# Kernel tuning notes

Measured on AMD Instinct MI355X. Metric: run time of the kernel, lower is better.

The kernel has to match this reference:

```python
import jax, jax.numpy as jnp
import numpy as np

B, S, D = 4, 2048, 1024  # batch, seq_len, input_dim == output_dim (dk)


def setup_inputs() -> dict:
    key = jax.random.key(0)
    kx, kq, kk, kv = jax.random.split(key, 4)
    # xavier_uniform bound for square [D, D] matrices
    bound = float(np.sqrt(6.0 / (D + D)))
    return {
        "x": jax.random.normal(kx, (B, S, D), dtype=jnp.float32),
        "WQ": jax.random.uniform(kq, (D, D), jnp.float32, -bound, bound),
        "WK": jax.random.uniform(kk, (D, D), jnp.float32, -bound, bound),
        "WV": jax.random.uniform(kv, (D, D), jnp.float32, -bound, bound),
    }


def reference(x, WQ, WK, WV):
    dk = WQ.shape[1]
    q = x @ WQ  # [B, S, dk]
    k = x @ WK
    v = x @ WV
    scores = jnp.einsum("bsd,btd->bst", q, k) / jnp.sqrt(jnp.asarray(dk, x.dtype))
    # causal mask: tril ones -> positions where mask==0 set to -inf
    s = x.shape[1]
    causal = jnp.tril(jnp.ones((s, s), dtype=bool))
    scores = jnp.where(causal[None, :, :], scores, jnp.asarray(-jnp.inf, x.dtype))
    attention = jax.nn.softmax(scores, axis=-1)
    # NOTE: original applies attention_dropout to `scores` post-softmax and
    # discards the result -> dead op; eval-mode output is attention @ v.
    return jnp.einsum("bst,btd->bsd", attention, v)
```

## Files before the change

### kernel.cpp

```cpp
#include <hip/hip_runtime.h>
#include <stdint.h>


typedef unsigned short u16;
typedef __attribute__((ext_vector_type(8))) short shortx8;
typedef __attribute__((ext_vector_type(4))) float floatx4;

static constexpr int BB = 4;
static constexpr int SS = 2048;
static constexpr int DD = 1024;

__device__ __forceinline__ u16 f2bf(float f) {
  union { float f; uint32_t u; } c; c.f = f;
  uint32_t u = c.u;
  return (u16)((u + 0x7fffu + ((u >> 16) & 1u)) >> 16);
}

__device__ __forceinline__ float bfhi2f(uint32_t u) {
  union { uint32_t u; float f; } c; c.u = u & 0xffff0000u; return c.f;
}
__device__ __forceinline__ float bflo2f(uint32_t u) {
  union { uint32_t u; float f; } c; c.u = u << 16; return c.f;
}

#define GLOAD_LDS16(g, l)                                                              \
  __builtin_amdgcn_global_load_lds((const __attribute__((address_space(1))) void*)(g), \
                                   (__attribute__((address_space(3))) void*)(l), 16, 0, 0)

__device__ __forceinline__ void gemm_core_128(
    const u16* __restrict__ A, const u16* __restrict__ Bt,
    int lda, int ldb, int m0, int n0, int kend, floatx4 acc[4][4])
{
  __shared__ u16 lA[128 * 64];
  __shared__ u16 lB[128 * 64];
  const int t = threadIdx.x;
  const int w = t >> 6, l = t & 63;
  const int wm = w >> 1, wn = w & 1;
  const int sr = l >> 3;
  const int scq = ((l & 7) ^ (l >> 3)) * 8;

#pragma unroll
  for (int i = 0; i < 4; ++i)
#pragma unroll
    for (int j = 0; j < 4; ++j)
      acc[i][j] = (floatx4){0.f, 0.f, 0.f, 0.f};

  const u16* Ab = A + (size_t)m0 * lda;
  const u16* Bb = Bt + (size_t)n0 * ldb;

  for (int k0 = 0; k0 < kend; k0 += 64) {
#pragma unroll
    for (int i = 0; i < 4; ++i) {
      const int row = w * 32 + i * 8;
      GLOAD_LDS16(Ab + (size_t)(row + sr) * lda + k0 + scq, &lA[row * 64]);
      GLOAD_LDS16(Bb + (size_t)(row + sr) * ldb + k0 + scq, &lB[row * 64]);
    }
    __syncthreads();

#pragma unroll
    for (int ks = 0; ks < 2; ++ks) {
      const int ca = ((ks * 4 + (l >> 4)) ^ (l & 7)) * 8;
      shortx8 af[4], bf[4];
#pragma unroll
      for (int i = 0; i < 4; ++i)
        af[i] = *(const shortx8*)&lA[(wm * 64 + i * 16 + (l & 15)) * 64 + ca];
#pragma unroll
      for (int i = 0; i < 4; ++i)
        bf[i] = *(const shortx8*)&lB[(wn * 64 + i * 16 + (l & 15)) * 64 + ca];
#pragma unroll
      for (int i = 0; i < 4; ++i)
#pragma unroll
        for (int j = 0; j < 4; ++j)
          acc[i][j] = __builtin_amdgcn_mfma_f32_16x16x32_bf16(af[i], bf[j], acc[i][j], 0, 0, 0);
    }
    __syncthreads();
  }
}

__global__ __launch_bounds__(256) void prep(const float* __restrict__ x,
                                            const float* __restrict__ WQ,
                                            const float* __restrict__ WK,
                                            const float* __restrict__ WV,
                                            u16* __restrict__ xb,
                                            u16* __restrict__ Wt) {
  __shared__ float tile[64][65];
  const int bid = blockIdx.x;
  const int t = threadIdx.x;
  if (bid < 8192) {
    const size_t i = (size_t)bid * 256 + t;
    float4 v = ((const float4*)x)[i];
    ushort4 o;
    o.x = f2bf(v.x); o.y = f2bf(v.y); o.z = f2bf(v.z); o.w = f2bf(v.w);
    ((ushort4*)xb)[i] = o;
    return;
  }
  const int r = bid - 8192;
  const int wsel = r >> 8;
  const int rr = r & 255;
  const int k0 = (rr >> 4) * 64, n0 = (rr & 15) * 64;
  const float* W = wsel == 0 ? WQ : (wsel == 1 ? WK : WV);
  const int tx = t & 63, ty = t >> 6;
#pragma unroll
  for (int i = 0; i < 16; ++i)
    tile[ty + i * 4][tx] = W[(size_t)(k0 + ty + i * 4) * DD + n0 + tx];
  __syncthreads();
  u16* dst = Wt + (size_t)wsel * DD * DD;
#pragma unroll
  for (int i = 0; i < 16; ++i)
    dst[(size_t)(n0 + ty + i * 4) * DD + k0 + tx] = f2bf(tile[tx][ty + i * 4]);
}

__global__ __launch_bounds__(256, 2) void qkv_gemm(const u16* __restrict__ x,
                                                   const u16* __restrict__ Wt,
                                                   u16* __restrict__ Q,
                                                   u16* __restrict__ K,
                                                   u16* __restrict__ Vt) {
  const int m0 = blockIdx.x * 128;
  const int n0t = blockIdx.y * 128;
  floatx4 acc[4][4];
  gemm_core_128(x, Wt, DD, DD, m0, n0t, DD, acc);

  const int t = threadIdx.x, w = t >> 6, l = t & 63;
  const int wm = w >> 1, wn = w & 1;

  if (n0t >= 2048) {
    const int bb = m0 >> 11;
    const int s0 = (m0 & 2047) + wm * 64 + (l >> 4) * 4;
    u16* vt = Vt + (size_t)bb * DD * SS;
#pragma unroll
    for (int i = 0; i < 4; ++i)
#pragma unroll
      for (int j = 0; j < 4; ++j) {
        const int n = (n0t - 2048) + wn * 64 + j * 16 + (l & 15);
        const int s = s0 + i * 16;
        ushort4 o4;
        o4.x = f2bf(acc[i][j][0]);
        o4.y = f2bf(acc[i][j][1]);
        o4.z = f2bf(acc[i][j][2]);
        o4.w = f2bf(acc[i][j][3]);
        *(ushort4*)(vt + (size_t)n * SS + s) = o4;
      }
    return;
  }

  u16* out = (n0t < 1024) ? Q : K;
  const int n0 = n0t & 1023;
#pragma unroll
  for (int i = 0; i < 4; ++i)
#pragma unroll
    for (int j = 0; j < 4; ++j)
#pragma unroll
      for (int r = 0; r < 4; ++r) {
        const int m = m0 + wm * 64 + i * 16 + (l >> 4) * 4 + r;
        const int n = n0 + wn * 64 + j * 16 + (l & 15);
        out[(size_t)m * DD + n] = f2bf(acc[i][j][r]);
      }
}

__global__ __launch_bounds__(256, 2) void scores_gemm(const u16* __restrict__ Q,
                                                      const u16* __restrict__ Kt,
                                                      u16* __restrict__ Scb) {
  const int b = blockIdx.z;
  const int tcode = blockIdx.x;
  int mb = (int)((sqrtf(8.0f * (float)tcode + 1.0f) - 1.0f) * 0.5f);
  while ((mb + 1) * (mb + 2) / 2 <= tcode) ++mb;
  while (mb * (mb + 1) / 2 > tcode) --mb;
  const int nb = tcode - mb * (mb + 1) / 2;
  const int m0 = mb * 128, n0 = nb * 128;

  floatx4 acc[4][4];
  gemm_core_128(Q + (size_t)b * SS * DD, Kt + (size_t)b * SS * DD, DD, DD, m0, n0, DD, acc);

  u16* out = Scb + (size_t)b * SS * SS;
  const int t = threadIdx.x, w = t >> 6, l = t & 63;
  const int wm = w >> 1, wn = w & 1;
#pragma unroll
  for (int i = 0; i < 4; ++i)
#pragma unroll
    for (int j = 0; j < 4; ++j)
#pragma unroll
      for (int r = 0; r < 4; ++r) {
        const int m = m0 + wm * 64 + i * 16 + (l >> 4) * 4 + r;
        const int n = n0 + wn * 64 + j * 16 + (l & 15);
        out[(size_t)m * SS + n] = f2bf(acc[i][j][r] * 0.03125f);
      }
}

__global__ __launch_bounds__(256) void softmax_causal(const u16* __restrict__ Scb,
                                                      u16* __restrict__ P) {
  const int row = blockIdx.x * 4 + (threadIdx.x >> 6);
  const int l = threadIdx.x & 63;
  const int b = row >> 11, i = row & 2047;
  const u16* s = Scb + (size_t)b * SS * SS + (size_t)i * SS;
  u16* p = P + (size_t)b * SS * SS + (size_t)i * SS;
  const int n = i + 1;
  const int jend = (i + 128) & ~127;
  const int nc = (jend + 511) >> 9;

  float v[4][8];
  float mx = -INFINITY;
#pragma unroll
  for (int c = 0; c < 4; ++c) {
    if (c < nc) {
      const int col = c * 512 + l * 8;
      uint4 raw = *(const uint4*)(s + col);
      v[c][0] = bflo2f(raw.x); v[c][1] = bfhi2f(raw.x);
      v[c][2] = bflo2f(raw.y); v[c][3] = bfhi2f(raw.y);
      v[c][4] = bflo2f(raw.z); v[c][5] = bfhi2f(raw.z);
      v[c][6] = bflo2f(raw.w); v[c][7] = bfhi2f(raw.w);
#pragma unroll
      for (int e = 0; e < 8; ++e) {
        v[c][e] = (col + e < n) ? v[c][e] : -INFINITY;
        mx = fmaxf(mx, v[c][e]);
      }
    }
  }
#pragma unroll
  for (int o = 32; o > 0; o >>= 1) mx = fmaxf(mx, __shfl_xor(mx, o, 64));

  float sum = 0.f;
#pragma unroll
  for (int c = 0; c < 4; ++c) {
    if (c < nc) {
#pragma unroll
      for (int e = 0; e < 8; ++e) {
        v[c][e] = __expf(v[c][e] - mx);
        sum += v[c][e];
      }
    }
  }
#pragma unroll
  for (int o = 32; o > 0; o >>= 1) sum += __shfl_xor(sum, o, 64);
  const float inv = 1.0f / sum;

#pragma unroll
  for (int c = 0; c < 4; ++c) {
    if (c < nc) {
      const int col = c * 512 + l * 8;
      if (col < jend) {
        uint4 o4;
        o4.x = (uint32_t)f2bf(v[c][0] * inv) | ((uint32_t)f2bf(v[c][1] * inv) << 16);
        o4.y = (uint32_t)f2bf(v[c][2] * inv) | ((uint32_t)f2bf(v[c][3] * inv) << 16);
        o4.z = (uint32_t)f2bf(v[c][4] * inv) | ((uint32_t)f2bf(v[c][5] * inv) << 16);
        o4.w = (uint32_t)f2bf(v[c][6] * inv) | ((uint32_t)f2bf(v[c][7] * inv) << 16);
        *(uint4*)(p + col) = o4;
      }
    }
  }
}

__global__ __launch_bounds__(256, 2) void pv_gemm(const u16* __restrict__ P,
                                                  const u16* __restrict__ Vt,
                                                  float* __restrict__ out) {
  const int b = blockIdx.z;
  const int mb = 15 - blockIdx.y;
  const int m0 = mb * 128, n0 = blockIdx.x * 128;
  floatx4 acc[4][4];
  gemm_core_128(P + (size_t)b * SS * SS, Vt + (size_t)b * DD * SS, SS, SS, m0, n0, m0 + 128, acc);

  float* o = out + (size_t)b * SS * DD;
  const int t = threadIdx.x, w = t >> 6, l = t & 63;
  const int wm = w >> 1, wn = w & 1;
#pragma unroll
  for (int i = 0; i < 4; ++i)
#pragma unroll
    for (int j = 0; j < 4; ++j)
#pragma unroll
      for (int r = 0; r < 4; ++r) {
        const int m = m0 + wm * 64 + i * 16 + (l >> 4) * 4 + r;
        const int n = n0 + wn * 64 + j * 16 + (l & 15);
        o[(size_t)m * DD + n] = acc[i][j][r];
      }
}

extern "C" void kernel_launch(void* const* d_in, const int* in_sizes, int n_in,
                              void* d_out, int out_size, void* d_ws, size_t ws_size,
                              hipStream_t stream) {
  const float* x  = (const float*)d_in[0];
  const float* WQ = (const float*)d_in[1];
  const float* WK = (const float*)d_in[2];
  const float* WV = (const float*)d_in[3];
  float* out = (float*)d_out;

  char* ws = (char*)d_ws;
  const size_t WT_OFF = 0;
  const size_t XB_OFF = WT_OFF + (size_t)3072 * 1024 * 2;
  const size_t Q_OFF  = XB_OFF + (size_t)BB * SS * DD * 2;
  const size_t K_OFF  = Q_OFF + (size_t)BB * SS * DD * 2;
  const size_t VT_OFF = K_OFF + (size_t)BB * SS * DD * 2;
  const size_t P_OFF  = VT_OFF + (size_t)BB * SS * DD * 2;
  const size_t SC_OFF = P_OFF + (size_t)BB * SS * SS * 2;
  u16* Wt  = (u16*)(ws + WT_OFF);
  u16* xb  = (u16*)(ws + XB_OFF);
  u16* Q   = (u16*)(ws + Q_OFF);
  u16* Kb  = (u16*)(ws + K_OFF);
  u16* Vt  = (u16*)(ws + VT_OFF);
  u16* P   = (u16*)(ws + P_OFF);
  u16* Scb = (u16*)(ws + SC_OFF);

  hipLaunchKernelGGL(prep, dim3(8960), dim3(256), 0, stream, x, WQ, WK, WV, xb, Wt);
  hipLaunchKernelGGL(qkv_gemm, dim3(64, 24), dim3(256), 0, stream, xb, Wt, Q, Kb, Vt);
  hipLaunchKernelGGL(scores_gemm, dim3(136, 1, 4), dim3(256), 0, stream, Q, Kb, Scb);
  hipLaunchKernelGGL(softmax_causal, dim3(2048), dim3(256), 0, stream, Scb, P);
  hipLaunchKernelGGL(pv_gemm, dim3(8, 16, 4), dim3(256), 0, stream, P, Vt, out);
}
```

Baseline: 236.6 us.

## Use 128x256 tiles for scores GEMM and split-K balance the PV GEMM

The scores GEMM now uses a 128x256 tile with a new triangular block enumeration, which halves the number of blocks and gives more reuse per block. The PV GEMM is rebalanced with a fixed 24-job table that splits long causal rows (mb>=8) into two K-ranges accumulated with atomicAdd. To make that accumulation start from zero, the softmax kernel now zeroes the lower-half output rows. The change aims to cut tail imbalance from the causal workload, at the cost of fp32 atomics, extra zeroing writes and a larger LDS and register footprint.

```diff
diff --git a/kernel.cpp b/kernel.cpp
--- a/kernel.cpp
+++ b/kernel.cpp
@@ -71,6 +71,60 @@
       for (int i = 0; i < 4; ++i)
 #pragma unroll
         for (int j = 0; j < 4; ++j)
+          acc[i][j] = __builtin_amdgcn_mfma_f32_16x16x32_bf16(af[i], bf[j], acc[i][j], 0, 0, 0);
+    }
+    __syncthreads();
+  }
+}
+
+__device__ __forceinline__ void gemm_core_128x256(
+    const u16* __restrict__ A, const u16* __restrict__ Bt,
+    int lda, int ldb, int m0, int n0, int kend, floatx4 acc[4][8])
+{
+  __shared__ u16 lA[128 * 64];
+  __shared__ u16 lB[256 * 64];
+  const int t = threadIdx.x;
+  const int w = t >> 6, l = t & 63;
+  const int wm = w >> 1, wn = w & 1;
+  const int sr = l >> 3;
+  const int scq = ((l & 7) ^ (l >> 3)) * 8;
+
+#pragma unroll
+  for (int i = 0; i < 4; ++i)
+#pragma unroll
+    for (int j = 0; j < 8; ++j)
+      acc[i][j] = (floatx4){0.f, 0.f, 0.f, 0.f};
+
+  const u16* Ab = A + (size_t)m0 * lda;
+  const u16* Bb = Bt + (size_t)n0 * ldb;
+
+  for (int k0 = 0; k0 < kend; k0 += 64) {
+#pragma unroll
+    for (int i = 0; i < 4; ++i) {
+      const int row = w * 32 + i * 8;
+      GLOAD_LDS16(Ab + (size_t)(row + sr) * lda + k0 + scq, &lA[row * 64]);
+    }
+#pragma unroll
+    for (int i = 0; i < 8; ++i) {
+      const int row = w * 64 + i * 8;
+      GLOAD_LDS16(Bb + (size_t)(row + sr) * ldb + k0 + scq, &lB[row * 64]);
+    }
+    __syncthreads();
+
+#pragma unroll
+    for (int ks = 0; ks < 2; ++ks) {
+      const int ca = ((ks * 4 + (l >> 4)) ^ (l & 7)) * 8;
+      shortx8 af[4], bf[8];
+#pragma unroll
+      for (int i = 0; i < 4; ++i)
+        af[i] = *(const shortx8*)&lA[(wm * 64 + i * 16 + (l & 15)) * 64 + ca];
+#pragma unroll
+      for (int j = 0; j < 8; ++j)
+        bf[j] = *(const shortx8*)&lB[(wn * 128 + j * 16 + (l & 15)) * 64 + ca];
+#pragma unroll
+      for (int i = 0; i < 4; ++i)
+#pragma unroll
+        for (int j = 0; j < 8; ++j)
           acc[i][j] = __builtin_amdgcn_mfma_f32_16x16x32_bf16(af[i], bf[j], acc[i][j], 0, 0, 0);
     }
     __syncthreads();
@@ -160,16 +214,15 @@
 __global__ __launch_bounds__(256, 2) void scores_gemm(const u16* __restrict__ Q,
                                                       const u16* __restrict__ Kt,
                                                       u16* __restrict__ Scb) {
-  const int b = blockIdx.z;
+  const int b = blockIdx.y;
   const int tcode = blockIdx.x;
-  int mb = (int)((sqrtf(8.0f * (float)tcode + 1.0f) - 1.0f) * 0.5f);
-  while ((mb + 1) * (mb + 2) / 2 <= tcode) ++mb;
-  while (mb * (mb + 1) / 2 > tcode) --mb;
-  const int nb = tcode - mb * (mb + 1) / 2;
-  const int m0 = mb * 128, n0 = nb * 128;
-
-  floatx4 acc[4][4];
-  gemm_core_128(Q + (size_t)b * SS * DD, Kt + (size_t)b * SS * DD, DD, DD, m0, n0, DD, acc);
+  int mb = 0, c = 0;
+  while (c + (mb >> 1) + 1 <= tcode) { c += (mb >> 1) + 1; ++mb; }
+  const int nb = tcode - c;
+  const int m0 = mb * 128, n0 = nb * 256;
+
+  floatx4 acc[4][8];
+  gemm_core_128x256(Q + (size_t)b * SS * DD, Kt + (size_t)b * SS * DD, DD, DD, m0, n0, DD, acc);
 
   u16* out = Scb + (size_t)b * SS * SS;
   const int t = threadIdx.x, w = t >> 6, l = t & 63;
@@ -177,17 +230,29 @@
 #pragma unroll
   for (int i = 0; i < 4; ++i)
 #pragma unroll
-    for (int j = 0; j < 4; ++j)
+    for (int j = 0; j < 8; ++j)
 #pragma unroll
       for (int r = 0; r < 4; ++r) {
         const int m = m0 + wm * 64 + i * 16 + (l >> 4) * 4 + r;
-        const int n = n0 + wn * 64 + j * 16 + (l & 15);
+        const int n = n0 + wn * 128 + j * 16 + (l & 15);
         out[(size_t)m * SS + n] = f2bf(acc[i][j][r] * 0.03125f);
       }
 }
 
 __global__ __launch_bounds__(256) void softmax_causal(const u16* __restrict__ Scb,
-                                                      u16* __restrict__ P) {
+                                                      u16* __restrict__ P,
+                                                      float* __restrict__ outz) {
+  {
+    float4* ov = (float4*)outz;
+    const int tid = blockIdx.x * 256 + threadIdx.x;
+#pragma unroll
+    for (int rep = 0; rep < 2; ++rep) {
+      const int z = tid * 2 + rep;
+      const int b = z >> 18, local = z & 262143;
+      ov[(size_t)b * 524288 + 262144 + local] = (float4){0.f, 0.f, 0.f, 0.f};
+    }
+  }
+
   const int row = blockIdx.x * 4 + (threadIdx.x >> 6);
   const int l = threadIdx.x & 63;
   const int b = row >> 11, i = row & 2047;
@@ -249,18 +314,34 @@
   }
 }
 
+__device__ const int jb_mb[24] = {  7,  8,  9, 10, 11, 12, 13, 14, 15, 15,
+                                    6, 14,  5, 13,  4, 12,  3, 11,  2, 10,
+                                    1,  9,  0,  8 };
+__device__ const int jb_k0[24] = {  0,  0,  0,  0,  0,  0,  0,  0,  0, 1024,
+                                    0, 1024, 0, 1024, 0, 1024, 0, 1024, 0, 1024,
+                                    0, 1024, 0, 1024 };
+__device__ const int jb_k1[24] = { 1024, 1024, 1024, 1024, 1024, 1024, 1024, 1024, 1024, 2048,
+                                   896, 1920, 768, 1792, 640, 1664, 512, 1536, 384, 1408,
+                                   256, 1280, 128, 1152 };
+
 __global__ __launch_bounds__(256, 2) void pv_gemm(const u16* __restrict__ P,
                                                   const u16* __restrict__ Vt,
                                                   float* __restrict__ out) {
-  const int b = blockIdx.z;
-  const int mb = 15 - blockIdx.y;
+  const int b = blockIdx.y;
+  const int job = blockIdx.z;
+  const int mb = jb_mb[job];
+  const int k0 = jb_k0[job], k1 = jb_k1[job];
   const int m0 = mb * 128, n0 = blockIdx.x * 128;
+
   floatx4 acc[4][4];
-  gemm_core_128(P + (size_t)b * SS * SS, Vt + (size_t)b * DD * SS, SS, SS, m0, n0, m0 + 128, acc);
+  gemm_core_128(P + (size_t)b * SS * SS + k0,
+                Vt + (size_t)b * DD * SS + k0,
+                SS, SS, m0, n0, k1 - k0, acc);
 
   float* o = out + (size_t)b * SS * DD;
   const int t = threadIdx.x, w = t >> 6, l = t & 63;
   const int wm = w >> 1, wn = w & 1;
+  const bool single = (mb < 8);
 #pragma unroll
   for (int i = 0; i < 4; ++i)
 #pragma unroll
@@ -269,7 +350,8 @@
       for (int r = 0; r < 4; ++r) {
         const int m = m0 + wm * 64 + i * 16 + (l >> 4) * 4 + r;
         const int n = n0 + wn * 64 + j * 16 + (l & 15);
-        o[(size_t)m * DD + n] = acc[i][j][r];
+        if (single) o[(size_t)m * DD + n] = acc[i][j][r];
+        else        atomicAdd(&o[(size_t)m * DD + n], acc[i][j][r]);
       }
 }
 
@@ -300,7 +382,7 @@
 
   hipLaunchKernelGGL(prep, dim3(8960), dim3(256), 0, stream, x, WQ, WK, WV, xb, Wt);
   hipLaunchKernelGGL(qkv_gemm, dim3(64, 24), dim3(256), 0, stream, xb, Wt, Q, Kb, Vt);
-  hipLaunchKernelGGL(scores_gemm, dim3(136, 1, 4), dim3(256), 0, stream, Q, Kb, Scb);
-  hipLaunchKernelGGL(softmax_causal, dim3(2048), dim3(256), 0, stream, Scb, P);
-  hipLaunchKernelGGL(pv_gemm, dim3(8, 16, 4), dim3(256), 0, stream, P, Vt, out);
-}
+  hipLaunchKernelGGL(scores_gemm, dim3(72, 4), dim3(256), 0, stream, Q, Kb, Scb);
+  hipLaunchKernelGGL(softmax_causal, dim3(2048), dim3(256), 0, stream, Scb, P, out);
+  hipLaunchKernelGGL(pv_gemm, dim3(8, 4, 24), dim3(256), 0, stream, P, Vt, out);
+}
```

Result: no change. 241.1 us (+1.9%).

## Fuse QKV, scores, softmax and PV into one cooperative persistent kernel

Applied to the files above, without the earlier changes.

Replaces the four separate launches after prep with a single cooperative kernel of 512 persistent blocks. The blocks loop over the tiles of each phase and are separated by grid-wide syncs. Shared LDS buffers are passed into the GEMM core, and a multi-kernel fallback runs if the cooperative launch fails. The aim is to remove per-launch overhead and the drain/fill gaps between kernels. In exchange it adds grid-barrier cost, drops the __restrict__ qualifiers, and drops the largest-first ordering of the PV tiles.

```diff
diff --git a/kernel.cpp b/kernel.cpp
--- a/kernel.cpp
+++ b/kernel.cpp
@@ -1,5 +1,8 @@
 #include <hip/hip_runtime.h>
+#include <hip/hip_cooperative_groups.h>
 #include <stdint.h>
+
+namespace cg = cooperative_groups;
 
 
 typedef unsigned short u16;
@@ -9,13 +12,13 @@
 static constexpr int BB = 4;
 static constexpr int SS = 2048;
 static constexpr int DD = 1024;
+static constexpr int NBLK = 512;
 
 __device__ __forceinline__ u16 f2bf(float f) {
   union { float f; uint32_t u; } c; c.f = f;
   uint32_t u = c.u;
   return (u16)((u + 0x7fffu + ((u >> 16) & 1u)) >> 16);
 }
-
 __device__ __forceinline__ float bfhi2f(uint32_t u) {
   union { uint32_t u; float f; } c; c.u = u & 0xffff0000u; return c.f;
 }
@@ -29,10 +32,9 @@
 
 __device__ __forceinline__ void gemm_core_128(
     const u16* __restrict__ A, const u16* __restrict__ Bt,
-    int lda, int ldb, int m0, int n0, int kend, floatx4 acc[4][4])
+    int lda, int ldb, int m0, int n0, int kend, floatx4 acc[4][4],
+    u16* lA, u16* lB)
 {
-  __shared__ u16 lA[128 * 64];
-  __shared__ u16 lB[128 * 64];
   const int t = threadIdx.x;
   const int w = t >> 6, l = t & 63;
   const int wm = w >> 1, wn = w & 1;
@@ -75,6 +77,215 @@
     }
     __syncthreads();
   }
+}
+
+
+__device__ __forceinline__ void phase_qkv(int bid, const u16* xb, const u16* Wt,
+                                          u16* Q, u16* K, u16* Vt,
+                                          u16* lA, u16* lB) {
+  const int t = threadIdx.x, w = t >> 6, l = t & 63;
+  const int wm = w >> 1, wn = w & 1;
+  for (int tid = bid; tid < 1536; tid += NBLK) {
+    const int m0 = (tid & 63) * 128;
+    const int n0t = (tid >> 6) * 128;
+    floatx4 acc[4][4];
+    gemm_core_128(xb, Wt, DD, DD, m0, n0t, DD, acc, lA, lB);
+
+    if (n0t >= 2048) {
+      const int bb = m0 >> 11;
+      const int s0 = (m0 & 2047) + wm * 64 + (l >> 4) * 4;
+      u16* vt = Vt + (size_t)bb * DD * SS;
+#pragma unroll
+      for (int i = 0; i < 4; ++i)
+#pragma unroll
+        for (int j = 0; j < 4; ++j) {
+          const int n = (n0t - 2048) + wn * 64 + j * 16 + (l & 15);
+          const int s = s0 + i * 16;
+          ushort4 o4;
+          o4.x = f2bf(acc[i][j][0]);
+          o4.y = f2bf(acc[i][j][1]);
+          o4.z = f2bf(acc[i][j][2]);
+          o4.w = f2bf(acc[i][j][3]);
+          *(ushort4*)(vt + (size_t)n * SS + s) = o4;
+        }
+      continue;
+    }
+
+    u16* out = (n0t < 1024) ? Q : K;
+    const int n0 = n0t & 1023;
+#pragma unroll
+    for (int i = 0; i < 4; ++i)
+#pragma unroll
+      for (int j = 0; j < 4; ++j)
+#pragma unroll
+        for (int r = 0; r < 4; ++r) {
+          const int m = m0 + wm * 64 + i * 16 + (l >> 4) * 4 + r;
+          const int n = n0 + wn * 64 + j * 16 + (l & 15);
+          out[(size_t)m * DD + n] = f2bf(acc[i][j][r]);
+        }
+  }
+}
+
+__device__ __forceinline__ void phase_scores(int bid, const u16* Q, const u16* Kt,
+                                             u16* Scb, u16* lA, u16* lB) {
+  const int t = threadIdx.x, w = t >> 6, l = t & 63;
+  const int wm = w >> 1, wn = w & 1;
+  for (int tt = bid; tt < 544; tt += NBLK) {
+    const int b = tt / 136;
+    const int tcode = tt - b * 136;
+    int mb = (int)((sqrtf(8.0f * (float)tcode + 1.0f) - 1.0f) * 0.5f);
+    while ((mb + 1) * (mb + 2) / 2 <= tcode) ++mb;
+    while (mb * (mb + 1) / 2 > tcode) --mb;
+    const int nb = tcode - mb * (mb + 1) / 2;
+    const int m0 = mb * 128, n0 = nb * 128;
+
+    floatx4 acc[4][4];
+    gemm_core_128(Q + (size_t)b * SS * DD, Kt + (size_t)b * SS * DD,
+                  DD, DD, m0, n0, DD, acc, lA, lB);
+
+    u16* out = Scb + (size_t)b * SS * SS;
+#pragma unroll
+    for (int i = 0; i < 4; ++i)
+#pragma unroll
+      for (int j = 0; j < 4; ++j)
+#pragma unroll
+        for (int r = 0; r < 4; ++r) {
+          const int m = m0 + wm * 64 + i * 16 + (l >> 4) * 4 + r;
+          const int n = n0 + wn * 64 + j * 16 + (l & 15);
+          out[(size_t)m * SS + n] = f2bf(acc[i][j][r] * 0.03125f);
+        }
+  }
+}
+
+__device__ __forceinline__ void phase_softmax(int bid, const u16* Scb, u16* P) {
+  const int wid = bid * 4 + (threadIdx.x >> 6);
+  const int l = threadIdx.x & 63;
+  for (int rep = 0; rep < 4; ++rep) {
+    const int row = wid + rep * 2048;
+    const int b = row >> 11, i = row & 2047;
+    const u16* s = Scb + (size_t)b * SS * SS + (size_t)i * SS;
+    u16* p = P + (size_t)b * SS * SS + (size_t)i * SS;
+    const int n = i + 1;
+    const int jend = (i + 128) & ~127;
+    const int nc = (jend + 511) >> 9;
+
+    float v[4][8];
+    float mx = -INFINITY;
+#pragma unroll
+    for (int c = 0; c < 4; ++c) {
+      if (c < nc) {
+        const int col = c * 512 + l * 8;
+        uint4 raw = *(const uint4*)(s + col);
+        v[c][0] = bflo2f(raw.x); v[c][1] = bfhi2f(raw.x);
+        v[c][2] = bflo2f(raw.y); v[c][3] = bfhi2f(raw.y);
+        v[c][4] = bflo2f(raw.z); v[c][5] = bfhi2f(raw.z);
+        v[c][6] = bflo2f(raw.w); v[c][7] = bfhi2f(raw.w);
+#pragma unroll
+        for (int e = 0; e < 8; ++e) {
+          v[c][e] = (col + e < n) ? v[c][e] : -INFINITY;
+          mx = fmaxf(mx, v[c][e]);
+        }
+      }
+    }
+#pragma unroll
+    for (int o = 32; o > 0; o >>= 1) mx = fmaxf(mx, __shfl_xor(mx, o, 64));
+
+    float sum = 0.f;
+#pragma unroll
+    for (int c = 0; c < 4; ++c) {
+      if (c < nc) {
+#pragma unroll
+        for (int e = 0; e < 8; ++e) {
+          v[c][e] = __expf(v[c][e] - mx);
+          sum += v[c][e];
+        }
+      }
+    }
+#pragma unroll
+    for (int o = 32; o > 0; o >>= 1) sum += __shfl_xor(sum, o, 64);
+    const float inv = 1.0f / sum;
+
+#pragma unroll
+    for (int c = 0; c < 4; ++c) {
+      if (c < nc) {
+        const int col = c * 512 + l * 8;
+        if (col < jend) {
+          uint4 o4;
+          o4.x = (uint32_t)f2bf(v[c][0] * inv) | ((uint32_t)f2bf(v[c][1] * inv) << 16);
+          o4.y = (uint32_t)f2bf(v[c][2] * inv) | ((uint32_t)f2bf(v[c][3] * inv) << 16);
+          o4.z = (uint32_t)f2bf(v[c][4] * inv) | ((uint32_t)f2bf(v[c][5] * inv) << 16);
+          o4.w = (uint32_t)f2bf(v[c][6] * inv) | ((uint32_t)f2bf(v[c][7] * inv) << 16);
+          *(uint4*)(p + col) = o4;
+        }
+      }
+    }
+  }
+}
+
+__device__ __forceinline__ void phase_pv(int bid, const u16* P, const u16* Vt,
+                                         float* out, u16* lA, u16* lB) {
+  const int b = bid >> 7;
+  const int r = bid & 127;
+  const int mb = r >> 3, n0 = (r & 7) * 128;
+  const int m0 = mb * 128;
+  floatx4 acc[4][4];
+  gemm_core_128(P + (size_t)b * SS * SS, Vt + (size_t)b * DD * SS,
+                SS, SS, m0, n0, m0 + 128, acc, lA, lB);
+
+  float* o = out + (size_t)b * SS * DD;
+  const int t = threadIdx.x, w = t >> 6, l = t & 63;
+  const int wm = w >> 1, wn = w & 1;
+#pragma unroll
+  for (int i = 0; i < 4; ++i)
+#pragma unroll
+    for (int j = 0; j < 4; ++j)
+#pragma unroll
+      for (int r2 = 0; r2 < 4; ++r2) {
+        const int m = m0 + wm * 64 + i * 16 + (l >> 4) * 4 + r2;
+        const int n = n0 + wn * 64 + j * 16 + (l & 15);
+        o[(size_t)m * DD + n] = acc[i][j][r2];
+      }
+}
+
+__global__ __launch_bounds__(256, 2) void mega(const u16* xb, const u16* Wt,
+                                               u16* Q, u16* K, u16* Vt,
+                                               u16* Scb, u16* P, float* out) {
+  __shared__ u16 lA[128 * 64];
+  __shared__ u16 lB[128 * 64];
+  cg::grid_group g = cg::this_grid();
+  const int bid = blockIdx.x;
+  phase_qkv(bid, xb, Wt, Q, K, Vt, lA, lB);
+  __threadfence();
+  g.sync();
+  phase_scores(bid, Q, K, Scb, lA, lB);
+  __threadfence();
+  g.sync();
+  phase_softmax(bid, Scb, P);
+  __threadfence();
+  g.sync();
+  phase_pv(bid, P, Vt, out, lA, lB);
+}
+
+__global__ __launch_bounds__(256, 2) void qkv_k(const u16* xb, const u16* Wt,
+                                                u16* Q, u16* K, u16* Vt) {
+  __shared__ u16 lA[128 * 64];
+  __shared__ u16 lB[128 * 64];
+  phase_qkv(blockIdx.x, xb, Wt, Q, K, Vt, lA, lB);
+}
+__global__ __launch_bounds__(256, 2) void scores_k(const u16* Q, const u16* Kt,
+                                                   u16* Scb) {
+  __shared__ u16 lA[128 * 64];
+  __shared__ u16 lB[128 * 64];
+  phase_scores(blockIdx.x, Q, Kt, Scb, lA, lB);
+}
+__global__ __launch_bounds__(256) void softmax_k(const u16* Scb, u16* P) {
+  phase_softmax(blockIdx.x, Scb, P);
+}
+__global__ __launch_bounds__(256, 2) void pv_k(const u16* P, const u16* Vt,
+                                               float* out) {
+  __shared__ u16 lA[128 * 64];
+  __shared__ u16 lB[128 * 64];
+  phase_pv(blockIdx.x, P, Vt, out, lA, lB);
 }
 
 __global__ __launch_bounds__(256) void prep(const float* __restrict__ x,
@@ -110,169 +321,6 @@
     dst[(size_t)(n0 + ty + i * 4) * DD + k0 + tx] = f2bf(tile[tx][ty + i * 4]);
 }
 
-__global__ __launch_bounds__(256, 2) void qkv_gemm(const u16* __restrict__ x,
-                                                   const u16* __restrict__ Wt,
-                                                   u16* __restrict__ Q,
-                                                   u16* __restrict__ K,
-                                                   u16* __restrict__ Vt) {
-  const int m0 = blockIdx.x * 128;
-  const int n0t = blockIdx.y * 128;
-  floatx4 acc[4][4];
-  gemm_core_128(x, Wt, DD, DD, m0, n0t, DD, acc);
-
-  const int t = threadIdx.x, w = t >> 6, l = t & 63;
-  const int wm = w >> 1, wn = w & 1;
-
-  if (n0t >= 2048) {
-    const int bb = m0 >> 11;
-    const int s0 = (m0 & 2047) + wm * 64 + (l >> 4) * 4;
-    u16* vt = Vt + (size_t)bb * DD * SS;
-#pragma unroll
-    for (int i = 0; i < 4; ++i)
-#pragma unroll
-      for (int j = 0; j < 4; ++j) {
-        const int n = (n0t - 2048) + wn * 64 + j * 16 + (l & 15);
-        const int s = s0 + i * 16;
-        ushort4 o4;
-        o4.x = f2bf(acc[i][j][0]);
-        o4.y = f2bf(acc[i][j][1]);
-        o4.z = f2bf(acc[i][j][2]);
-        o4.w = f2bf(acc[i][j][3]);
-        *(ushort4*)(vt + (size_t)n * SS + s) = o4;
-      }
-    return;
-  }
-
-  u16* out = (n0t < 1024) ? Q : K;
-  const int n0 = n0t & 1023;
-#pragma unroll
-  for (int i = 0; i < 4; ++i)
-#pragma unroll
-    for (int j = 0; j < 4; ++j)
-#pragma unroll
-      for (int r = 0; r < 4; ++r) {
-        const int m = m0 + wm * 64 + i * 16 + (l >> 4) * 4 + r;
-        const int n = n0 + wn * 64 + j * 16 + (l & 15);
-        out[(size_t)m * DD + n] = f2bf(acc[i][j][r]);
-      }
-}
-
-__global__ __launch_bounds__(256, 2) void scores_gemm(const u16* __restrict__ Q,
-                                                      const u16* __restrict__ Kt,
-                                                      u16* __restrict__ Scb) {
-  const int b = blockIdx.z;
-  const int tcode = blockIdx.x;
-  int mb = (int)((sqrtf(8.0f * (float)tcode + 1.0f) - 1.0f) * 0.5f);
-  while ((mb + 1) * (mb + 2) / 2 <= tcode) ++mb;
-  while (mb * (mb + 1) / 2 > tcode) --mb;
-  const int nb = tcode - mb * (mb + 1) / 2;
-  const int m0 = mb * 128, n0 = nb * 128;
-
-  floatx4 acc[4][4];
-  gemm_core_128(Q + (size_t)b * SS * DD, Kt + (size_t)b * SS * DD, DD, DD, m0, n0, DD, acc);
-
-  u16* out = Scb + (size_t)b * SS * SS;
-  const int t = threadIdx.x, w = t >> 6, l = t & 63;
-  const int wm = w >> 1, wn = w & 1;
-#pragma unroll
-  for (int i = 0; i < 4; ++i)
-#pragma unroll
-    for (int j = 0; j < 4; ++j)
-#pragma unroll
-      for (int r = 0; r < 4; ++r) {
-        const int m = m0 + wm * 64 + i * 16 + (l >> 4) * 4 + r;
-        const int n = n0 + wn * 64 + j * 16 + (l & 15);
-        out[(size_t)m * SS + n] = f2bf(acc[i][j][r] * 0.03125f);
-      }
-}
-
-__global__ __launch_bounds__(256) void softmax_causal(const u16* __restrict__ Scb,
-                                                      u16* __restrict__ P) {
-  const int row = blockIdx.x * 4 + (threadIdx.x >> 6);
-  const int l = threadIdx.x & 63;
-  const int b = row >> 11, i = row & 2047;
-  const u16* s = Scb + (size_t)b * SS * SS + (size_t)i * SS;
-  u16* p = P + (size_t)b * SS * SS + (size_t)i * SS;
-  const int n = i + 1;
-  const int jend = (i + 128) & ~127;
-  const int nc = (jend + 511) >> 9;
-
-  float v[4][8];
-  float mx = -INFINITY;
-#pragma unroll
-  for (int c = 0; c < 4; ++c) {
-    if (c < nc) {
-      const int col = c * 512 + l * 8;
-      uint4 raw = *(const uint4*)(s + col);
-      v[c][0] = bflo2f(raw.x); v[c][1] = bfhi2f(raw.x);
-      v[c][2] = bflo2f(raw.y); v[c][3] = bfhi2f(raw.y);
-      v[c][4] = bflo2f(raw.z); v[c][5] = bfhi2f(raw.z);
-      v[c][6] = bflo2f(raw.w); v[c][7] = bfhi2f(raw.w);
-#pragma unroll
-      for (int e = 0; e < 8; ++e) {
-        v[c][e] = (col + e < n) ? v[c][e] : -INFINITY;
-        mx = fmaxf(mx, v[c][e]);
-      }
-    }
-  }
-#pragma unroll
-  for (int o = 32; o > 0; o >>= 1) mx = fmaxf(mx, __shfl_xor(mx, o, 64));
-
-  float sum = 0.f;
-#pragma unroll
-  for (int c = 0; c < 4; ++c) {
-    if (c < nc) {
-#pragma unroll
-      for (int e = 0; e < 8; ++e) {
-        v[c][e] = __expf(v[c][e] - mx);
-        sum += v[c][e];
-      }
-    }
-  }
-#pragma unroll
-  for (int o = 32; o > 0; o >>= 1) sum += __shfl_xor(sum, o, 64);
-  const float inv = 1.0f / sum;
-
-#pragma unroll
-  for (int c = 0; c < 4; ++c) {
-    if (c < nc) {
-      const int col = c * 512 + l * 8;
-      if (col < jend) {
-        uint4 o4;
-        o4.x = (uint32_t)f2bf(v[c][0] * inv) | ((uint32_t)f2bf(v[c][1] * inv) << 16);
-        o4.y = (uint32_t)f2bf(v[c][2] * inv) | ((uint32_t)f2bf(v[c][3] * inv) << 16);
-        o4.z = (uint32_t)f2bf(v[c][4] * inv) | ((uint32_t)f2bf(v[c][5] * inv) << 16);
-        o4.w = (uint32_t)f2bf(v[c][6] * inv) | ((uint32_t)f2bf(v[c][7] * inv) << 16);
-        *(uint4*)(p + col) = o4;
-      }
-    }
-  }
-}
-
-__global__ __launch_bounds__(256, 2) void pv_gemm(const u16* __restrict__ P,
-                                                  const u16* __restrict__ Vt,
-                                                  float* __restrict__ out) {
-  const int b = blockIdx.z;
-  const int mb = 15 - blockIdx.y;
-  const int m0 = mb * 128, n0 = blockIdx.x * 128;
-  floatx4 acc[4][4];
-  gemm_core_128(P + (size_t)b * SS * SS, Vt + (size_t)b * DD * SS, SS, SS, m0, n0, m0 + 128, acc);
-
-  float* o = out + (size_t)b * SS * DD;
-  const int t = threadIdx.x, w = t >> 6, l = t & 63;
-  const int wm = w >> 1, wn = w & 1;
-#pragma unroll
-  for (int i = 0; i < 4; ++i)
-#pragma unroll
-    for (int j = 0; j < 4; ++j)
-#pragma unroll
-      for (int r = 0; r < 4; ++r) {
-        const int m = m0 + wm * 64 + i * 16 + (l >> 4) * 4 + r;
-        const int n = n0 + wn * 64 + j * 16 + (l & 15);
-        o[(size_t)m * DD + n] = acc[i][j][r];
-      }
-}
-
 extern "C" void kernel_launch(void* const* d_in, const int* in_sizes, int n_in,
                               void* d_out, int out_size, void* d_ws, size_t ws_size,
                               hipStream_t stream) {
@@ -299,8 +347,15 @@
   u16* Scb = (u16*)(ws + SC_OFF);
 
   hipLaunchKernelGGL(prep, dim3(8960), dim3(256), 0, stream, x, WQ, WK, WV, xb, Wt);
-  hipLaunchKernelGGL(qkv_gemm, dim3(64, 24), dim3(256), 0, stream, xb, Wt, Q, Kb, Vt);
-  hipLaunchKernelGGL(scores_gemm, dim3(136, 1, 4), dim3(256), 0, stream, Q, Kb, Scb);
-  hipLaunchKernelGGL(softmax_causal, dim3(2048), dim3(256), 0, stream, Scb, P);
-  hipLaunchKernelGGL(pv_gemm, dim3(8, 16, 4), dim3(256), 0, stream, P, Vt, out);
-}
+
+  void* args[8] = {(void*)&xb, (void*)&Wt, (void*)&Q, (void*)&Kb,
+                   (void*)&Vt, (void*)&Scb, (void*)&P, (void*)&out};
+  hipError_t e = hipLaunchCooperativeKernel((void*)mega, dim3(NBLK), dim3(256),
+                                            args, 0, stream);
+  if (e != hipSuccess) {
+    hipLaunchKernelGGL(qkv_k, dim3(NBLK), dim3(256), 0, stream, xb, Wt, Q, Kb, Vt);
+    hipLaunchKernelGGL(scores_k, dim3(NBLK), dim3(256), 0, stream, Q, Kb, Scb);
+    hipLaunchKernelGGL(softmax_k, dim3(NBLK), dim3(256), 0, stream, Scb, P);
+    hipLaunchKernelGGL(pv_k, dim3(NBLK), dim3(256), 0, stream, P, Vt, out);
+  }
+}
```

Measured after the change: 623.3 us. 163% more time.
